# Optimization experiments

Hardware: AMD Instinct MI355X
Metric: run time of the kernel (lower is better)

## Reference

```python
import jax, jax.numpy as jnp
import numpy as np

EPS = 1e-5
G = 8    # groups
K = 3    # kernel_size


def bn(x, gamma, beta, mean, var):
    # inference-mode BatchNorm2d; x: (b,C,H,W), params: (C,)
    inv = gamma / jnp.sqrt(var + EPS)
    return x * inv[None, :, None, None] + (beta - mean * inv)[None, :, None, None]


def gconv1x1(x, w):
    # grouped 1x1 conv; x: (b, g*ci, H, W), w: (g, co, ci) -> (b, g*co, H, W)
    b, C, H, W = x.shape
    g, co, ci = w.shape
    xg = x.reshape(b, g, ci, H, W)
    y = jnp.einsum('bgihw,goi->bgohw', xg, w)
    return y.reshape(b, g * co, H, W)


def unfold3(x):
    # torch.nn.Unfold(k=3, stride=1, dilation=1, padding=1), reshaped to (b, C, 9, H, W)
    b, C, H, W = x.shape
    xp = jnp.pad(x, ((0, 0), (0, 0), (1, 1), (1, 1)))
    patches = [xp[:, :, i:i + H, j:j + W] for i in range(K) for j in range(K)]
    return jnp.stack(patches, axis=2)


def setup_inputs() -> dict:
    key = jax.random.key(0)
    ks = jax.random.split(key, 16)
    f = jax.random.normal
    u = jax.random.uniform
    return {
        'x':  f(ks[0], (2, 256, 128, 128), jnp.float32),
        'w1': f(ks[1], (8, 8, 32), jnp.float32) * 0.1,
        'b1': f(ks[2], (64,), jnp.float32) * 0.1,
        'g1': u(ks[3], (64,), jnp.float32, 0.5, 1.5),
        'be1': f(ks[4], (64,), jnp.float32) * 0.1,
        'm1': f(ks[5], (64,), jnp.float32) * 0.1,
        'v1': u(ks[6], (64,), jnp.float32, 0.5, 1.5),
        'w2': f(ks[7], (8, 10, 8), jnp.float32) * 0.1,
        'b2': f(ks[8], (80,), jnp.float32) * 0.1,
        'g2': u(ks[9], (80,), jnp.float32, 0.5, 1.5),
        'be2': f(ks[10], (80,), jnp.float32) * 0.1,
        'm2': f(ks[11], (80,), jnp.float32) * 0.1,
        'v2': u(ks[12], (80,), jnp.float32, 0.5, 1.5),
        'wv': f(ks[13], (8, 32, 32), jnp.float32) * 0.1,
    }


def reference(x, w1, b1, g1, be1, m1, v1, w2, b2, g2, be2, m2, v2, wv):
    b, C, H, W = x.shape
    # mask_conv: grouped 1x1 conv -> BN -> tanh -> grouped 1x1 conv -> BN
    t = jnp.tanh(bn(gconv1x1(x, w1) + b1[None, :, None, None], g1, be1, m1, v1))
    mn = bn(gconv1x1(t, w2) + b2[None, :, None, None], g2, be2, m2, v2)  # (b, G*(1+K*K), H, W)
    neighbor = mn[:, :G]          # (b, G, H, W)
    mask = mn[:, G:]              # (b, G*K*K, H, W)
    nb = unfold3(neighbor)        # (b, G, 9, H, W)
    logits = mask.reshape(b, G, K * K, H, W) + nb
    attn = jax.nn.softmax(logits, axis=2)               # (b, G, 9, H, W)
    # value path: grouped 1x1 conv (no bias) then unfold
    v = gconv1x1(x, wv)                                  # (b, C, H, W)
    vu = unfold3(v).reshape(b, G, C // G, K * K, H, W)   # (b, G, C/G, 9, H, W)
    out = jnp.einsum('bgkhw,bgckhw->bgchw', attn, vu)    # weighted sum over window
    return out.reshape(b, C, H, W)
```

## Files before the change

kernel.cpp:

```cpp
#include <hip/hip_runtime.h>
#include <hip/hip_bf16.h>

#define HW  16384
#define WD  128

#define TS   16
#define HS   18
#define HP   (HS * HS)
#define PRS  20
#define PLS  360

__device__ __forceinline__ unsigned short f2bf(float f) {
    unsigned int u = __builtin_bit_cast(unsigned int, f);
    u += 0x7FFFu + ((u >> 16) & 1u);
    return (unsigned short)(u >> 16);
}
__device__ __forceinline__ float bf2f(unsigned short s) {
    return __builtin_bit_cast(float, (unsigned int)s << 16);
}
__device__ __forceinline__ float ftanh(float v) {
    const float e = __expf(2.0f * v);
    return 1.0f - __fdividef(2.0f, e + 1.0f);
}

__global__ __launch_bounds__(256) void la_fused(
    const float* __restrict__ x,
    const float* __restrict__ w1, const float* __restrict__ b1,
    const float* __restrict__ g1, const float* __restrict__ be1,
    const float* __restrict__ m1, const float* __restrict__ v1,
    const float* __restrict__ w2, const float* __restrict__ b2,
    const float* __restrict__ g2, const float* __restrict__ be2,
    const float* __restrict__ m2, const float* __restrict__ v2,
    const float* __restrict__ wv,
    float* __restrict__ out)
{
    __shared__ ushort4 vt[8 * PLS];
    __shared__ float   nbs[PLS];

    const int tid  = threadIdx.x;
    const int bg   = blockIdx.x;
    const int tile = blockIdx.y;
    const int b    = bg >> 3, g = bg & 7;
    const int ty0  = (tile >> 3) * TS;
    const int tx0  = (tile & 7) * TS;

    const float* xg  = x + (size_t)(b * 256 + g * 32) * HW;
    const float* x0  = x + (size_t)(b * 256) * HW;
    const float* wvg = wv + g * 1024;

    const float inv_nb = g2[g] * rsqrtf(v2[g] + 1e-5f);
    const float add_nb = be2[g] + (b2[g] - m2[g]) * inv_nb;

    for (int hp = tid; hp < HP; hp += 256) {
        const int hy = hp / HS, hx = hp - hy * HS;
        const int iy = ty0 + hy - 1, ix = tx0 + hx - 1;
        const int slot = hy * PRS + hx;
        if (((unsigned)iy < 128u) && ((unsigned)ix < 128u)) {
            const int po = iy * WD + ix;
            float xv[32], xz[32];
#pragma unroll
            for (int c = 0; c < 32; ++c) xv[c] = xg[(size_t)c * HW + po];
#pragma unroll
            for (int c = 0; c < 32; ++c) xz[c] = x0[(size_t)c * HW + po];

#pragma unroll
            for (int o4 = 0; o4 < 8; ++o4) {
                float a0 = 0.f, a1 = 0.f, a2 = 0.f, a3 = 0.f;
                const float* wp = wvg + o4 * 128;
#pragma unroll
                for (int c = 0; c < 32; ++c) {
                    const float xc = xv[c];
                    a0 = fmaf(xc, wp[c],      a0);
                    a1 = fmaf(xc, wp[32 + c], a1);
                    a2 = fmaf(xc, wp[64 + c], a2);
                    a3 = fmaf(xc, wp[96 + c], a3);
                }
                vt[o4 * PLS + slot] = make_ushort4(f2bf(a0), f2bf(a1), f2bf(a2), f2bf(a3));
            }

            float accn = 0.f;
#pragma unroll
            for (int o = 0; o < 8; ++o) {
                float a = 0.f;
#pragma unroll
                for (int ci = 0; ci < 32; ++ci) a = fmaf(xz[ci], w1[o * 32 + ci], a);
                const float inv = g1[o] * rsqrtf(v1[o] + 1e-5f);
                const float add = be1[o] + (b1[o] - m1[o]) * inv;
                const float t0 = ftanh(fmaf(a, inv, add));
                accn = fmaf(t0, w2[g * 8 + o], accn);
            }
            nbs[slot] = fmaf(accn, inv_nb, add_nb);
        } else {
            const ushort4 z = make_ushort4(0, 0, 0, 0);
#pragma unroll
            for (int o4 = 0; o4 < 8; ++o4) vt[o4 * PLS + slot] = z;
            nbs[slot] = 0.f;
        }
    }
    __syncthreads();

    const int cy  = tid >> 4, cx = tid & 15;
    const int iy  = ty0 + cy, ix = tx0 + cx;
    const int pix = iy * WD + ix;

    const int mc0    = 8 + 9 * g;
    const int pa     = mc0 / 10;
    const int pb     = (mc0 + 8) / 10;
    const int ksplit = 10 - (mc0 - pa * 10);

    float tA[8], tB[8];
    {
        const float* xp  = x  + (size_t)(b * 256 + pa * 32) * HW + pix;
        const float* w1p = w1 + pa * 256;
        float xv[32];
#pragma unroll
        for (int c = 0; c < 32; ++c) xv[c] = xp[(size_t)c * HW];
#pragma unroll
        for (int o = 0; o < 8; ++o) {
            float a = 0.f;
#pragma unroll
            for (int ci = 0; ci < 32; ++ci) a = fmaf(xv[ci], w1p[o * 32 + ci], a);
            const int ch = pa * 8 + o;
            const float inv = g1[ch] * rsqrtf(v1[ch] + 1e-5f);
            const float add = be1[ch] + (b1[ch] - m1[ch]) * inv;
            tA[o] = ftanh(fmaf(a, inv, add));
        }
    }
    if (pb != pa) {
        const float* xp  = x  + (size_t)(b * 256 + pb * 32) * HW + pix;
        const float* w1p = w1 + pb * 256;
        float xv[32];
#pragma unroll
        for (int c = 0; c < 32; ++c) xv[c] = xp[(size_t)c * HW];
#pragma unroll
        for (int o = 0; o < 8; ++o) {
            float a = 0.f;
#pragma unroll
            for (int ci = 0; ci < 32; ++ci) a = fmaf(xv[ci], w1p[o * 32 + ci], a);
            const int ch = pb * 8 + o;
            const float inv = g1[ch] * rsqrtf(v1[ch] + 1e-5f);
            const float add = be1[ch] + (b1[ch] - m1[ch]) * inv;
            tB[o] = ftanh(fmaf(a, inv, add));
        }
    } else {
#pragma unroll
        for (int o = 0; o < 8; ++o) tB[o] = tA[o];
    }

    float lg[9];
    float mx = -1e30f;
#pragma unroll
    for (int k = 0; k < 9; ++k) {
        const int mc = mc0 + k;
        const int p  = (k < ksplit) ? pa : pb;
        const int o  = mc - p * 10;
        const float* w2p = w2 + p * 80 + o * 8;
        float a = 0.f;
#pragma unroll
        for (int i = 0; i < 8; ++i) {
            const float ti = (k < ksplit) ? tA[i] : tB[i];
            a = fmaf(ti, w2p[i], a);
        }
        const float inv = g2[mc] * rsqrtf(v2[mc] + 1e-5f);
        const float add = be2[mc] + (b2[mc] - m2[mc]) * inv;
        const float mask = fmaf(a, inv, add);
        lg[k] = mask + nbs[(cy + k / 3) * PRS + (cx + k % 3)];
        mx = fmaxf(mx, lg[k]);
    }
    float s = 0.f;
#pragma unroll
    for (int k = 0; k < 9; ++k) { lg[k] = __expf(lg[k] - mx); s += lg[k]; }
    const float rs = 1.f / s;
#pragma unroll
    for (int k = 0; k < 9; ++k) lg[k] *= rs;

    float* og = out + (size_t)(b * 256 + g * 32) * HW + pix;
#pragma unroll 2
    for (int o4 = 0; o4 < 8; ++o4) {
        const ushort4* vp = vt + o4 * PLS;
        float a0 = 0.f, a1 = 0.f, a2 = 0.f, a3 = 0.f;
#pragma unroll
        for (int k = 0; k < 9; ++k) {
            const int slot = (cy + k / 3) * PRS + (cx + k % 3);
            const ushort4 vv = vp[slot];
            a0 = fmaf(lg[k], bf2f(vv.x), a0);
            a1 = fmaf(lg[k], bf2f(vv.y), a1);
            a2 = fmaf(lg[k], bf2f(vv.z), a2);
            a3 = fmaf(lg[k], bf2f(vv.w), a3);
        }
        __builtin_nontemporal_store(a0, og + (size_t)(o4 * 4 + 0) * HW);
        __builtin_nontemporal_store(a1, og + (size_t)(o4 * 4 + 1) * HW);
        __builtin_nontemporal_store(a2, og + (size_t)(o4 * 4 + 2) * HW);
        __builtin_nontemporal_store(a3, og + (size_t)(o4 * 4 + 3) * HW);
    }
}

extern "C" void kernel_launch(void* const* d_in, const int* in_sizes, int n_in,
                              void* d_out, int out_size, void* d_ws, size_t ws_size,
                              hipStream_t stream)
{
    const float* x   = (const float*)d_in[0];
    const float* w1  = (const float*)d_in[1];
    const float* b1  = (const float*)d_in[2];
    const float* g1  = (const float*)d_in[3];
    const float* be1 = (const float*)d_in[4];
    const float* m1  = (const float*)d_in[5];
    const float* v1  = (const float*)d_in[6];
    const float* w2  = (const float*)d_in[7];
    const float* b2  = (const float*)d_in[8];
    const float* g2  = (const float*)d_in[9];
    const float* be2 = (const float*)d_in[10];
    const float* m2  = (const float*)d_in[11];
    const float* v2  = (const float*)d_in[12];
    const float* wv  = (const float*)d_in[13];

    float* out = (float*)d_out;

    dim3 blk(256);
    dim3 grd(16, 64);

    hipLaunchKernelGGL(la_fused, grd, blk, 0, stream,
                       x, w1, b1, g1, be1, m1, v1, w2, b2, g2, be2, m2, v2, wv,
                       out);
}
```

Before: 142.0 us.

## Precompute neighbor logits in a separate kernel instead of per-group halo recompute

A new pre-pass kernel computes the 8 neighbor channels (first grouped conv, BN, tanh, second conv, BN) once per pixel and writes them to workspace. Before, every one of the 8 group blocks recomputed them over the halo tile, reading an extra 32 input channels per pixel. The fused kernel now loads those values from the workspace. It also swaps the grid dimensions so consecutive blocks walk tiles within one batch-group, and adds a launch-bounds occupancy hint of 4. The cost is an extra launch and a global round trip of 8 channels per batch.

```diff
diff --git a/kernel.cpp b/kernel.cpp
--- a/kernel.cpp
+++ b/kernel.cpp
@@ -23,7 +23,7 @@
     return 1.0f - __fdividef(2.0f, e + 1.0f);
 }
 
-__global__ __launch_bounds__(256) void la_fused(
+__global__ __launch_bounds__(256) void la_nb(
     const float* __restrict__ x,
     const float* __restrict__ w1, const float* __restrict__ b1,
     const float* __restrict__ g1, const float* __restrict__ be1,
@@ -31,25 +31,63 @@
     const float* __restrict__ w2, const float* __restrict__ b2,
     const float* __restrict__ g2, const float* __restrict__ be2,
     const float* __restrict__ m2, const float* __restrict__ v2,
-    const float* __restrict__ wv,
+    float* __restrict__ nb)
+{
+    const int pix = blockIdx.x * blockDim.x + threadIdx.x;
+    const int b   = blockIdx.y;
+
+    const float* xp = x + (size_t)(b * 256) * HW + pix;
+    float xv[32];
+#pragma unroll
+    for (int c = 0; c < 32; ++c) xv[c] = xp[(size_t)c * HW];
+
+    float t0[8];
+#pragma unroll
+    for (int o = 0; o < 8; ++o) {
+        float a = 0.f;
+#pragma unroll
+        for (int ci = 0; ci < 32; ++ci) a = fmaf(xv[ci], w1[o * 32 + ci], a);
+        const float inv = g1[o] * rsqrtf(v1[o] + 1e-5f);
+        const float add = be1[o] + (b1[o] - m1[o]) * inv;
+        t0[o] = ftanh(fmaf(a, inv, add));
+    }
+
+    float* np = nb + (size_t)(b * 8) * HW + pix;
+#pragma unroll
+    for (int o = 0; o < 8; ++o) {
+        float a = 0.f;
+#pragma unroll
+        for (int i = 0; i < 8; ++i) a = fmaf(t0[i], w2[o * 8 + i], a);
+        const float inv = g2[o] * rsqrtf(v2[o] + 1e-5f);
+        const float add = be2[o] + (b2[o] - m2[o]) * inv;
+        np[(size_t)o * HW] = fmaf(a, inv, add);
+    }
+}
+
+__global__ __launch_bounds__(256, 4) void la_fused(
+    const float* __restrict__ x,
+    const float* __restrict__ w1, const float* __restrict__ b1,
+    const float* __restrict__ g1, const float* __restrict__ be1,
+    const float* __restrict__ m1, const float* __restrict__ v1,
+    const float* __restrict__ w2, const float* __restrict__ b2,
+    const float* __restrict__ g2, const float* __restrict__ be2,
+    const float* __restrict__ m2, const float* __restrict__ v2,
+    const float* __restrict__ wv, const float* __restrict__ nb,
     float* __restrict__ out)
 {
     __shared__ ushort4 vt[8 * PLS];
     __shared__ float   nbs[PLS];
 
     const int tid  = threadIdx.x;
-    const int bg   = blockIdx.x;
-    const int tile = blockIdx.y;
+    const int tile = blockIdx.x;
+    const int bg   = blockIdx.y;
     const int b    = bg >> 3, g = bg & 7;
     const int ty0  = (tile >> 3) * TS;
     const int tx0  = (tile & 7) * TS;
 
-    const float* xg  = x + (size_t)(b * 256 + g * 32) * HW;
-    const float* x0  = x + (size_t)(b * 256) * HW;
+    const float* xg  = x  + (size_t)(b * 256 + g * 32) * HW;
     const float* wvg = wv + g * 1024;
-
-    const float inv_nb = g2[g] * rsqrtf(v2[g] + 1e-5f);
-    const float add_nb = be2[g] + (b2[g] - m2[g]) * inv_nb;
+    const float* nbp = nb + (size_t)(b * 8 + g) * HW;
 
     for (int hp = tid; hp < HP; hp += 256) {
         const int hy = hp / HS, hx = hp - hy * HS;
@@ -57,12 +95,10 @@
         const int slot = hy * PRS + hx;
         if (((unsigned)iy < 128u) && ((unsigned)ix < 128u)) {
             const int po = iy * WD + ix;
-            float xv[32], xz[32];
+            float xv[32];
 #pragma unroll
             for (int c = 0; c < 32; ++c) xv[c] = xg[(size_t)c * HW + po];
-#pragma unroll
-            for (int c = 0; c < 32; ++c) xz[c] = x0[(size_t)c * HW + po];
-
+            nbs[slot] = nbp[po];
 #pragma unroll
             for (int o4 = 0; o4 < 8; ++o4) {
                 float a0 = 0.f, a1 = 0.f, a2 = 0.f, a3 = 0.f;
@@ -77,19 +113,6 @@
                 }
                 vt[o4 * PLS + slot] = make_ushort4(f2bf(a0), f2bf(a1), f2bf(a2), f2bf(a3));
             }
-
-            float accn = 0.f;
-#pragma unroll
-            for (int o = 0; o < 8; ++o) {
-                float a = 0.f;
-#pragma unroll
-                for (int ci = 0; ci < 32; ++ci) a = fmaf(xz[ci], w1[o * 32 + ci], a);
-                const float inv = g1[o] * rsqrtf(v1[o] + 1e-5f);
-                const float add = be1[o] + (b1[o] - m1[o]) * inv;
-                const float t0 = ftanh(fmaf(a, inv, add));
-                accn = fmaf(t0, w2[g * 8 + o], accn);
-            }
-            nbs[slot] = fmaf(accn, inv_nb, add_nb);
         } else {
             const ushort4 z = make_ushort4(0, 0, 0, 0);
 #pragma unroll
@@ -215,11 +238,15 @@
     const float* wv  = (const float*)d_in[13];
 
     float* out = (float*)d_out;
+    float* nb  = (float*)d_ws;
 
     dim3 blk(256);
-    dim3 grd(16, 64);
-
+    dim3 gnb(HW / 256, 2);
+    dim3 grd(64, 16);
+
+    hipLaunchKernelGGL(la_nb, gnb, blk, 0, stream,
+                       x, w1, b1, g1, be1, m1, v1, w2, b2, g2, be2, m2, v2, nb);
     hipLaunchKernelGGL(la_fused, grd, blk, 0, stream,
                        x, w1, b1, g1, be1, m1, v1, w2, b2, g2, be2, m2, v2, wv,
-                       out);
-}
+                       nb, out);
+}
```

After: 152.8 us. 7.6% more time.

## Precompute tanh features in prepass and apply value conv after window aggregation

Applied to the files above, without the earlier changes.

Adds a prepass kernel that computes the first grouped conv, BN and tanh once per pixel and stores it as bf16 in the workspace. It also writes the neighbor logits, which removes the redundant per-halo and per-group recomputation in the main kernel. The main kernel now stages raw x as bf16 in shared memory and does the softmax-weighted 3x3 aggregation first. It then applies the 32x32 value conv once per output pixel instead of per halo pixel, using the linearity of the 1x1 conv. The cost is an extra launch and a global round trip for t and nb, bf16 rounding of t, and more register pressure from the 32-wide accumulator.

```diff
diff --git a/kernel.cpp b/kernel.cpp
--- a/kernel.cpp
+++ b/kernel.cpp
@@ -15,15 +15,15 @@
     u += 0x7FFFu + ((u >> 16) & 1u);
     return (unsigned short)(u >> 16);
 }
-__device__ __forceinline__ float bf2f(unsigned short s) {
-    return __builtin_bit_cast(float, (unsigned int)s << 16);
+__device__ __forceinline__ float bf2f(unsigned int s) {
+    return __builtin_bit_cast(float, (s & 0xFFFFu) << 16);
 }
 __device__ __forceinline__ float ftanh(float v) {
     const float e = __expf(2.0f * v);
     return 1.0f - __fdividef(2.0f, e + 1.0f);
 }
 
-__global__ __launch_bounds__(256) void la_fused(
+__global__ __launch_bounds__(256) void la_t(
     const float* __restrict__ x,
     const float* __restrict__ w1, const float* __restrict__ b1,
     const float* __restrict__ g1, const float* __restrict__ be1,
@@ -31,10 +31,60 @@
     const float* __restrict__ w2, const float* __restrict__ b2,
     const float* __restrict__ g2, const float* __restrict__ be2,
     const float* __restrict__ m2, const float* __restrict__ v2,
+    unsigned short* __restrict__ t, float* __restrict__ nb)
+{
+    const int pix = blockIdx.x * blockDim.x + threadIdx.x;
+    const int b   = blockIdx.y;
+    const int p   = blockIdx.z;
+
+    const float* xp = x + (size_t)(b * 256 + p * 32) * HW + pix;
+    float xv[32];
+#pragma unroll
+    for (int c = 0; c < 32; ++c) xv[c] = xp[(size_t)c * HW];
+
+    const float* w1p = w1 + p * 256;
+    float tv[8];
+#pragma unroll
+    for (int o = 0; o < 8; ++o) {
+        float a = 0.f;
+#pragma unroll
+        for (int ci = 0; ci < 32; ++ci) a = fmaf(xv[ci], w1p[o * 32 + ci], a);
+        const int ch = p * 8 + o;
+        const float inv = g1[ch] * rsqrtf(v1[ch] + 1e-5f);
+        const float add = be1[ch] + (b1[ch] - m1[ch]) * inv;
+        tv[o] = ftanh(fmaf(a, inv, add));
+    }
+
+    uint4 u;
+    u.x = (unsigned)f2bf(tv[0]) | ((unsigned)f2bf(tv[1]) << 16);
+    u.y = (unsigned)f2bf(tv[2]) | ((unsigned)f2bf(tv[3]) << 16);
+    u.z = (unsigned)f2bf(tv[4]) | ((unsigned)f2bf(tv[5]) << 16);
+    u.w = (unsigned)f2bf(tv[6]) | ((unsigned)f2bf(tv[7]) << 16);
+    *(uint4*)(t + ((size_t)(b * 8 + p) * HW + pix) * 8) = u;
+
+    if (p == 0) {
+#pragma unroll
+        for (int o = 0; o < 8; ++o) {
+            float a = 0.f;
+#pragma unroll
+            for (int i = 0; i < 8; ++i) a = fmaf(tv[i], w2[o * 8 + i], a);
+            const float inv = g2[o] * rsqrtf(v2[o] + 1e-5f);
+            const float add = be2[o] + (b2[o] - m2[o]) * inv;
+            nb[(size_t)(b * 8 + o) * HW + pix] = fmaf(a, inv, add);
+        }
+    }
+}
+
+__global__ __launch_bounds__(256, 4) void la_fused(
+    const float* __restrict__ x,
+    const float* __restrict__ w2, const float* __restrict__ b2,
+    const float* __restrict__ g2, const float* __restrict__ be2,
+    const float* __restrict__ m2, const float* __restrict__ v2,
     const float* __restrict__ wv,
+    const unsigned short* __restrict__ t, const float* __restrict__ nb,
     float* __restrict__ out)
 {
-    __shared__ ushort4 vt[8 * PLS];
+    __shared__ ushort4 xt[8 * PLS];
     __shared__ float   nbs[PLS];
 
     const int tid  = threadIdx.x;
@@ -44,12 +94,8 @@
     const int ty0  = (tile >> 3) * TS;
     const int tx0  = (tile & 7) * TS;
 
-    const float* xg  = x + (size_t)(b * 256 + g * 32) * HW;
-    const float* x0  = x + (size_t)(b * 256) * HW;
-    const float* wvg = wv + g * 1024;
-
-    const float inv_nb = g2[g] * rsqrtf(v2[g] + 1e-5f);
-    const float add_nb = be2[g] + (b2[g] - m2[g]) * inv_nb;
+    const float* xg  = x  + (size_t)(b * 256 + g * 32) * HW;
+    const float* nbp = nb + (size_t)(b * 8 + g) * HW;
 
     for (int hp = tid; hp < HP; hp += 256) {
         const int hy = hp / HS, hx = hp - hy * HS;
@@ -57,43 +103,19 @@
         const int slot = hy * PRS + hx;
         if (((unsigned)iy < 128u) && ((unsigned)ix < 128u)) {
             const int po = iy * WD + ix;
-            float xv[32], xz[32];
+            float xv[32];
 #pragma unroll
             for (int c = 0; c < 32; ++c) xv[c] = xg[(size_t)c * HW + po];
-#pragma unroll
-            for (int c = 0; c < 32; ++c) xz[c] = x0[(size_t)c * HW + po];
-
-#pragma unroll
-            for (int o4 = 0; o4 < 8; ++o4) {
-                float a0 = 0.f, a1 = 0.f, a2 = 0.f, a3 = 0.f;
-                const float* wp = wvg + o4 * 128;
-#pragma unroll
-                for (int c = 0; c < 32; ++c) {
-                    const float xc = xv[c];
-                    a0 = fmaf(xc, wp[c],      a0);
-                    a1 = fmaf(xc, wp[32 + c], a1);
-                    a2 = fmaf(xc, wp[64 + c], a2);
-                    a3 = fmaf(xc, wp[96 + c], a3);
-                }
-                vt[o4 * PLS + slot] = make_ushort4(f2bf(a0), f2bf(a1), f2bf(a2), f2bf(a3));
-            }
-
-            float accn = 0.f;
-#pragma unroll
-            for (int o = 0; o < 8; ++o) {
-                float a = 0.f;
-#pragma unroll
-                for (int ci = 0; ci < 32; ++ci) a = fmaf(xz[ci], w1[o * 32 + ci], a);
-                const float inv = g1[o] * rsqrtf(v1[o] + 1e-5f);
-                const float add = be1[o] + (b1[o] - m1[o]) * inv;
-                const float t0 = ftanh(fmaf(a, inv, add));
-                accn = fmaf(t0, w2[g * 8 + o], accn);
-            }
-            nbs[slot] = fmaf(accn, inv_nb, add_nb);
+            nbs[slot] = nbp[po];
+#pragma unroll
+            for (int c4 = 0; c4 < 8; ++c4)
+                xt[c4 * PLS + slot] = make_ushort4(
+                    f2bf(xv[c4 * 4 + 0]), f2bf(xv[c4 * 4 + 1]),
+                    f2bf(xv[c4 * 4 + 2]), f2bf(xv[c4 * 4 + 3]));
         } else {
             const ushort4 z = make_ushort4(0, 0, 0, 0);
 #pragma unroll
-            for (int o4 = 0; o4 < 8; ++o4) vt[o4 * PLS + slot] = z;
+            for (int c4 = 0; c4 < 8; ++c4) xt[c4 * PLS + slot] = z;
             nbs[slot] = 0.f;
         }
     }
@@ -110,38 +132,18 @@
 
     float tA[8], tB[8];
     {
-        const float* xp  = x  + (size_t)(b * 256 + pa * 32) * HW + pix;
-        const float* w1p = w1 + pa * 256;
-        float xv[32];
-#pragma unroll
-        for (int c = 0; c < 32; ++c) xv[c] = xp[(size_t)c * HW];
-#pragma unroll
-        for (int o = 0; o < 8; ++o) {
-            float a = 0.f;
-#pragma unroll
-            for (int ci = 0; ci < 32; ++ci) a = fmaf(xv[ci], w1p[o * 32 + ci], a);
-            const int ch = pa * 8 + o;
-            const float inv = g1[ch] * rsqrtf(v1[ch] + 1e-5f);
-            const float add = be1[ch] + (b1[ch] - m1[ch]) * inv;
-            tA[o] = ftanh(fmaf(a, inv, add));
-        }
+        const uint4 ua = *(const uint4*)(t + ((size_t)(b * 8 + pa) * HW + pix) * 8);
+        tA[0] = bf2f(ua.x); tA[1] = bf2f(ua.x >> 16);
+        tA[2] = bf2f(ua.y); tA[3] = bf2f(ua.y >> 16);
+        tA[4] = bf2f(ua.z); tA[5] = bf2f(ua.z >> 16);
+        tA[6] = bf2f(ua.w); tA[7] = bf2f(ua.w >> 16);
     }
     if (pb != pa) {
-        const float* xp  = x  + (size_t)(b * 256 + pb * 32) * HW + pix;
-        const float* w1p = w1 + pb * 256;
-        float xv[32];
-#pragma unroll
-        for (int c = 0; c < 32; ++c) xv[c] = xp[(size_t)c * HW];
-#pragma unroll
-        for (int o = 0; o < 8; ++o) {
-            float a = 0.f;
-#pragma unroll
-            for (int ci = 0; ci < 32; ++ci) a = fmaf(xv[ci], w1p[o * 32 + ci], a);
-            const int ch = pb * 8 + o;
-            const float inv = g1[ch] * rsqrtf(v1[ch] + 1e-5f);
-            const float add = be1[ch] + (b1[ch] - m1[ch]) * inv;
-            tB[o] = ftanh(fmaf(a, inv, add));
-        }
+        const uint4 ub = *(const uint4*)(t + ((size_t)(b * 8 + pb) * HW + pix) * 8);
+        tB[0] = bf2f(ub.x); tB[1] = bf2f(ub.x >> 16);
+        tB[2] = bf2f(ub.y); tB[3] = bf2f(ub.y >> 16);
+        tB[4] = bf2f(ub.z); tB[5] = bf2f(ub.z >> 16);
+        tB[6] = bf2f(ub.w); tB[7] = bf2f(ub.w >> 16);
     } else {
 #pragma unroll
         for (int o = 0; o < 8; ++o) tB[o] = tA[o];
@@ -163,35 +165,40 @@
         }
         const float inv = g2[mc] * rsqrtf(v2[mc] + 1e-5f);
         const float add = be2[mc] + (b2[mc] - m2[mc]) * inv;
-        const float mask = fmaf(a, inv, add);
-        lg[k] = mask + nbs[(cy + k / 3) * PRS + (cx + k % 3)];
+        lg[k] = fmaf(a, inv, add) + nbs[(cy + k / 3) * PRS + (cx + k % 3)];
         mx = fmaxf(mx, lg[k]);
     }
-    float s = 0.f;
-#pragma unroll
-    for (int k = 0; k < 9; ++k) { lg[k] = __expf(lg[k] - mx); s += lg[k]; }
-    const float rs = 1.f / s;
-#pragma unroll
-    for (int k = 0; k < 9; ++k) lg[k] *= rs;
-
+    float ssum = 0.f;
+#pragma unroll
+    for (int k = 0; k < 9; ++k) { lg[k] = __expf(lg[k] - mx); ssum += lg[k]; }
+    const float rs = 1.f / ssum;
+
+    float s[32];
+#pragma unroll
+    for (int c = 0; c < 32; ++c) s[c] = 0.f;
+#pragma unroll
+    for (int k = 0; k < 9; ++k) {
+        const int slot = (cy + k / 3) * PRS + (cx + k % 3);
+        const float e = lg[k];
+#pragma unroll
+        for (int c4 = 0; c4 < 8; ++c4) {
+            const ushort4 xv4 = xt[c4 * PLS + slot];
+            s[c4 * 4 + 0] = fmaf(e, bf2f(xv4.x), s[c4 * 4 + 0]);
+            s[c4 * 4 + 1] = fmaf(e, bf2f(xv4.y), s[c4 * 4 + 1]);
+            s[c4 * 4 + 2] = fmaf(e, bf2f(xv4.z), s[c4 * 4 + 2]);
+            s[c4 * 4 + 3] = fmaf(e, bf2f(xv4.w), s[c4 * 4 + 3]);
+        }
+    }
+
+    const float* wvg = wv + g * 1024;
     float* og = out + (size_t)(b * 256 + g * 32) * HW + pix;
-#pragma unroll 2
-    for (int o4 = 0; o4 < 8; ++o4) {
-        const ushort4* vp = vt + o4 * PLS;
-        float a0 = 0.f, a1 = 0.f, a2 = 0.f, a3 = 0.f;
-#pragma unroll
-        for (int k = 0; k < 9; ++k) {
-            const int slot = (cy + k / 3) * PRS + (cx + k % 3);
-            const ushort4 vv = vp[slot];
-            a0 = fmaf(lg[k], bf2f(vv.x), a0);
-            a1 = fmaf(lg[k], bf2f(vv.y), a1);
-            a2 = fmaf(lg[k], bf2f(vv.z), a2);
-            a3 = fmaf(lg[k], bf2f(vv.w), a3);
-        }
-        __builtin_nontemporal_store(a0, og + (size_t)(o4 * 4 + 0) * HW);
-        __builtin_nontemporal_store(a1, og + (size_t)(o4 * 4 + 1) * HW);
-        __builtin_nontemporal_store(a2, og + (size_t)(o4 * 4 + 2) * HW);
-        __builtin_nontemporal_store(a3, og + (size_t)(o4 * 4 + 3) * HW);
+#pragma unroll 4
+    for (int o = 0; o < 32; ++o) {
+        const float* wp = wvg + o * 32;
+        float a = 0.f;
+#pragma unroll
+        for (int ci = 0; ci < 32; ++ci) a = fmaf(s[ci], wp[ci], a);
+        __builtin_nontemporal_store(a * rs, og + (size_t)o * HW);
     }
 }
 
@@ -215,11 +222,16 @@
     const float* wv  = (const float*)d_in[13];
 
     float* out = (float*)d_out;
+    unsigned short* t = (unsigned short*)d_ws;
+    float* nb = (float*)(t + (size_t)2 * 8 * HW * 8);
 
     dim3 blk(256);
+    dim3 gt(HW / 256, 2, 8);
     dim3 grd(16, 64);
 
+    hipLaunchKernelGGL(la_t, gt, blk, 0, stream,
+                       x, w1, b1, g1, be1, m1, v1, w2, b2, g2, be2, m2, v2,
+                       t, nb);
     hipLaunchKernelGGL(la_fused, grd, blk, 0, stream,
-                       x, w1, b1, g1, be1, m1, v1, w2, b2, g2, be2, m2, v2, wv,
-                       out);
-}
+                       x, w2, b2, g2, be2, m2, v2, wv, t, nb, out);
+}
```

Result: faster. 130.6 us (-8.0%).
